# Kernel tuning notes

Hardware: AMD Instinct MI355X
Metric: run time of the kernel (lower is better)

The kernel has to match this reference:

```python
import jax, jax.numpy as jnp
import numpy as np
import math

N_HEAD = 12

def alibi_slopes(h):
    x = (2 ** 8) ** (1.0 / h)
    return jnp.array([1.0 / x ** (i + 1) for i in range(h)], dtype=jnp.float32)

def setup_inputs() -> dict:
    key = jax.random.key(0)
    k0, k1, k2 = jax.random.split(key, 3)
    B, T, C = 4, 2048, 576
    x = jax.random.normal(k0, (B, T, C), dtype=jnp.float32)
    w_qkv = jax.random.normal(k1, (3 * C, C), dtype=jnp.float32) * 0.02
    w_proj = jax.random.normal(k2, (C, C), dtype=jnp.float32) * 0.02
    return {"x": x, "w_qkv": w_qkv, "w_proj": w_proj}

def reference(x, w_qkv, w_proj):
    B, T, C = x.shape
    H = N_HEAD
    D = C // H
    qkv = x @ w_qkv.T  # [B,T,3C]
    q, k, v = jnp.split(qkv, 3, axis=2)
    q = q.reshape(B, T, H, D).transpose(0, 2, 1, 3)  # [B,H,T,D]
    k = k.reshape(B, T, H, D).transpose(0, 2, 1, 3)
    v = v.reshape(B, T, H, D).transpose(0, 2, 1, 3)
    # value residual with v1=None: v = 0.5*v + 0.5*v = v (faithful no-op)
    scale = 1.0 / math.sqrt(D)
    att = jnp.einsum('bhid,bhjd->bhij', q, k) * scale  # [B,H,T,T]
    # ALiBi bias as written: (col - row).clamp(min=0) * slope (zero on causal part)
    col = jnp.arange(T, dtype=jnp.float32)[None, :]
    row = jnp.arange(T, dtype=jnp.float32)[:, None]
    bias = jnp.maximum(col - row, 0.0)[None, :, :] * alibi_slopes(H)[:, None, None]  # [H,T,T]
    att = att + bias[None]
    causal = (jnp.arange(T)[None, :] <= jnp.arange(T)[:, None])  # [T,T] lower-tri
    att = jnp.where(causal[None, None], att, -jnp.inf)
    att = jax.nn.softmax(att, axis=-1)
    y = jnp.einsum('bhij,bhjd->bhid', att, v)  # [B,H,T,D]
    y = y.transpose(0, 2, 1, 3).reshape(B, T, C)
    return y @ w_proj.T
```

## Files before the change

### kernel.cpp

```cpp
#include <hip/hip_runtime.h>
#include <math.h>

#define Bn 4
#define Tn 2048
#define Cn 576
#define Hn 12
#define Dn 48
#define Mn (Bn*Tn)

#define QSCALE (1.4426950408889634f * 0.14433756729740643f)

typedef short  short8  __attribute__((ext_vector_type(8)));
typedef float  floatx4 __attribute__((ext_vector_type(4)));
typedef unsigned short ushort_t;
typedef unsigned short ushort8_t __attribute__((ext_vector_type(8)));

static __device__ __forceinline__ unsigned short f2bf(float f) {
    union { float f; unsigned int u; } v; v.f = f;
    unsigned int r = v.u + 0x7FFFu + ((v.u >> 16) & 1u);
    return (unsigned short)(r >> 16);
}

static __device__ __forceinline__ unsigned int pack_trunc(float a, float b) {
    union { float f; unsigned int u; } ua, ub; ua.f = a; ub.f = b;
    return (ua.u >> 16) | (ub.u & 0xFFFF0000u);
}

static __device__ __forceinline__ void gload16(void* lds, const void* g) {
    __builtin_amdgcn_global_load_lds(
        (const __attribute__((address_space(1))) void*)g,
        (__attribute__((address_space(3))) void*)lds, 16, 0, 0);
}

template<int N> static __device__ __forceinline__ void wait_vm_lg() {
    if constexpr (N == 0)
        asm volatile("s_waitcnt vmcnt(0) lgkmcnt(0)" ::: "memory");
    else if constexpr (N == 3)
        asm volatile("s_waitcnt vmcnt(3) lgkmcnt(0)" ::: "memory");
    else if constexpr (N == 5)
        asm volatile("s_waitcnt vmcnt(5) lgkmcnt(0)" ::: "memory");
    else if constexpr (N == 6)
        asm volatile("s_waitcnt vmcnt(6) lgkmcnt(0)" ::: "memory");
    else if constexpr (N == 10)
        asm volatile("s_waitcnt vmcnt(10) lgkmcnt(0)" ::: "memory");
    else
        static_assert(N == -12345, "unsupported waitcnt immediate");
}

__global__ __launch_bounds__(256)
void cast3(const float* __restrict__ a, ushort_t* __restrict__ oa, int na4,
           const float* __restrict__ b, ushort_t* __restrict__ ob, int nb4,
           const float* __restrict__ c, ushort_t* __restrict__ oc, int nc4)
{
    int i = blockIdx.x * 256 + threadIdx.x;
    const float* src; ushort_t* dst; int idx;
    if (i < na4)                  { src = a; dst = oa; idx = i; }
    else if (i < na4 + nb4)       { src = b; dst = ob; idx = i - na4; }
    else if (i < na4 + nb4 + nc4) { src = c; dst = oc; idx = i - na4 - nb4; }
    else return;
    float4 v = ((const float4*)src)[idx];
    ushort4 o;
    o.x = f2bf(v.x); o.y = f2bf(v.y); o.z = f2bf(v.z); o.w = f2bf(v.w);
    ((ushort4*)dst)[idx] = o;
}

template<int MODE, int MTILE>
__global__ __launch_bounds__(256)
void gemm_mfma(const ushort_t* __restrict__ A, const ushort_t* __restrict__ W,
               ushort_t* __restrict__ outb, float* __restrict__ outf)
{
    constexpr int SA   = MTILE / 16;
    constexpr int NSEG = SA + 4;
    constexpr int PW   = NSEG / 4;
    constexpr int MF   = MTILE / 64;
    constexpr int NB   = (MODE == 0) ? 27 : 9;
    constexpr int NST  = Cn / 32;
    constexpr int AH   = 3;
    constexpr int NBUF = 4;
    __shared__ __align__(16) ushort_t Ls[NBUF][NSEG][512];

    const int tid  = threadIdx.x;
    const int wave = tid >> 6;
    const int lane = tid & 63;
    const int m    = lane & 15;
    const int g    = lane >> 4;
    const int bid  = blockIdx.x;
    const int xcd  = bid & 7;
    const int slot = bid >> 3;
    const int n0   = (slot % NB) * 64;
    const int m0   = (xcd + 8 * (slot / NB)) * MTILE;

    floatx4 acc[MF][4];
    #pragma unroll
    for (int i = 0; i < MF; ++i)
        #pragma unroll
        for (int j = 0; j < 4; ++j)
            acc[i][j] = (floatx4){0.f, 0.f, 0.f, 0.f};

    const char* gp[PW];
    int         si[PW];
    #pragma unroll
    for (int i = 0; i < PW; ++i) {
        int s = wave + i * 4;
        si[i] = s;
        gp[i] = (s < SA)
            ? (const char*)(A + (size_t)(m0 + s * 16 + m) * Cn + g * 8)
            : (const char*)(W + (size_t)(n0 + (s - SA) * 16 + m) * Cn + g * 8);
    }

    #pragma unroll
    for (int s = 0; s < AH; ++s)
        #pragma unroll
        for (int i = 0; i < PW; ++i) { gload16(&Ls[s][si[i]][0], gp[i]); gp[i] += 64; }
    wait_vm_lg<(AH - 1) * PW>();
    __builtin_amdgcn_s_barrier();

    for (int j = 0; j < NST; ++j) {
        if (j + AH < NST) {
            #pragma unroll
            for (int i = 0; i < PW; ++i) {
                gload16(&Ls[(j + AH) & (NBUF - 1)][si[i]][0], gp[i]);
                gp[i] += 64;
            }
        }
        const int buf = j & (NBUF - 1);
        short8 bf4[4];
        #pragma unroll
        for (int jj = 0; jj < 4; ++jj)
            bf4[jj] = *(const short8*)&Ls[buf][SA + jj][lane * 8];
        #pragma unroll
        for (int i = 0; i < MF; ++i) {
            short8 af = *(const short8*)&Ls[buf][wave * MF + i][lane * 8];
            #pragma unroll
            for (int jj = 0; jj < 4; ++jj)
                acc[i][jj] = __builtin_amdgcn_mfma_f32_16x16x32_bf16(af, bf4[jj], acc[i][jj], 0, 0, 0);
        }
        if (j < NST - AH)        wait_vm_lg<(AH - 1) * PW>();
        else if (j == NST - AH)  wait_vm_lg<(AH - 2) * PW>();
        else                     wait_vm_lg<0>();
        __builtin_amdgcn_s_barrier();
    }

    const size_t per = (size_t)Bn * Hn * Tn * Dn;
    if (MODE == 0) {
        const int which = n0 / Cn;
        const int nb    = n0 - which * Cn;
        const int b     = m0 >> 11;
        const int t0g   = m0 & 2047;
        ushort_t* Lc = (ushort_t*)&Ls[0][0][0];
        if (which == 2) {
            constexpr int RS = MTILE + 8;
            #pragma unroll
            for (int i = 0; i < MF; ++i)
                #pragma unroll
                for (int j = 0; j < 4; ++j) {
                    ushort4 pk;
                    pk.x = f2bf(acc[i][j][0]); pk.y = f2bf(acc[i][j][1]);
                    pk.z = f2bf(acc[i][j][2]); pk.w = f2bf(acc[i][j][3]);
                    *(ushort4*)&Lc[(j * 16 + m) * RS + wave * (MTILE / 4) + i * 16 + g * 4] = pk;
                }
            __syncthreads();
            constexpr int CPC = MTILE / 8;
            constexpr int NIT = 64 * CPC / 256;
            #pragma unroll
            for (int it = 0; it < NIT; ++it) {
                int c    = tid + it * 256;
                int col  = c / CPC;
                int rowc = (c - col * CPC) * 8;
                int n    = nb + col;
                int h    = n / 48;
                int d    = n - h * 48;
                ushort_t* dst = outb + 2 * per
                    + (((size_t)(b * Hn + h) * Dn + d) * Tn) + t0g + rowc;
                *(ushort8_t*)dst = *(const ushort8_t*)&Lc[col * RS + rowc];
            }
        } else {
            const float sc = (which == 0) ? QSCALE : 1.0f;
            #pragma unroll
            for (int i = 0; i < MF; ++i)
                #pragma unroll
                for (int j = 0; j < 4; ++j)
                    #pragma unroll
                    for (int r = 0; r < 4; ++r)
                        Lc[(wave * (MTILE / 4) + i * 16 + g * 4 + r) * 80 + j * 16 + m] =
                            f2bf(acc[i][j][r] * sc);
            __syncthreads();
            constexpr int NIT = MTILE * 8 / 256;
            #pragma unroll
            for (int it = 0; it < NIT; ++it) {
                int c   = tid + it * 256;
                int row = c >> 3;
                int c8  = (c & 7) * 8;
                int n   = nb + c8;
                int h   = n / 48;
                int d   = n - h * 48;
                ushort_t* dst = outb + (size_t)which * per
                    + (((size_t)(b * Hn + h) * Tn + t0g + row) * Dn) + d;
                *(ushort8_t*)dst = *(const ushort8_t*)&Lc[row * 80 + c8];
            }
        }
    } else {
        #pragma unroll
        for (int i = 0; i < MF; ++i) {
            #pragma unroll
            for (int r = 0; r < 4; ++r) {
                int mrow = m0 + wave * (MTILE / 4) + i * 16 + g * 4 + r;
                #pragma unroll
                for (int j = 0; j < 4; ++j)
                    outf[(size_t)mrow * Cn + n0 + j * 16 + m] = acc[i][j][r];
            }
        }
    }
}

__global__ __launch_bounds__(512, 6)
void attn_mfma(const ushort_t* __restrict__ Q, const ushort_t* __restrict__ K,
               const ushort_t* __restrict__ V, ushort_t* __restrict__ Y,
               const ushort_t* __restrict__ zb)
{
    __shared__ __align__(16) ushort_t QPs[16][512];
    __shared__ __align__(16) ushort_t Ks[2][8][512];
    __shared__ __align__(16) ushort_t Vs[2][6][512];

    const int id   = blockIdx.x;
    const int kk   = id / 48;
    const int bh   = id - kk * 48;
    const int QT   = (kk & 1) ? (kk >> 1) : (15 - (kk >> 1));
    const int tid  = threadIdx.x;
    const int wave = tid >> 6;
    const int lane = tid & 63;
    const int m    = lane & 15;
    const int g    = lane >> 4;
    const int q0   = QT * 128;
    const int nkt  = 2 * QT + 2;

    const ushort_t* Qp = Q + (size_t)bh * Tn * Dn;
    const ushort_t* Kp = K + (size_t)bh * Tn * Dn;
    const ushort_t* Vp = V + (size_t)bh * Dn * Tn;

    {
        const char* qrp = (const char*)(Qp + (size_t)(q0 + wave * 16 + m) * Dn);
        gload16(&QPs[wave * 2 + 0][0], qrp + g * 16);
        gload16(&QPs[wave * 2 + 1][0], (g < 2) ? (qrp + 64 + g * 16) : (const char*)zb);
    }

    const bool  kpad = ((wave & 1) == 1) && (g >= 2);
    const char* kptr = kpad ? (const char*)zb
        : (const char*)(Kp + (size_t)((wave >> 1) * 16 + m) * Dn) + (wave & 1) * 64 + g * 16;
    const int   kadv = kpad ? 0 : 64 * Dn * 2;
    const char* vptr = (const char*)(Vp + (size_t)((wave >> 1) * 16 + m) * Tn)
                       + (wave & 1) * 64 + g * 16;
    const int   vadv = 64 * 2;

    gload16(&Ks[0][wave][0], kptr); kptr += kadv;
    if (wave < 6) { gload16(&Vs[0][wave][0], vptr); vptr += vadv; }
    __syncthreads();

    short8 bq[2];
    bq[0] = *(const short8*)&QPs[wave * 2 + 0][lane * 8];
    bq[1] = *(const short8*)&QPs[wave * 2 + 1][lane * 8];

    floatx4 acc[3];
    #pragma unroll
    for (int t = 0; t < 3; ++t) acc[t] = (floatx4){0.f, 0.f, 0.f, 0.f};
    float l_tot = 0.f;
    const int qrow  = q0 + wave * 16 + m;
    const int qwmin = q0 + wave * 16;
    const int qwmax = qwmin + 15;

    for (int jt = 0; jt < nkt; ++jt) {
        const int cur = jt & 1;
        const int j0  = jt * 64;
        if (jt + 1 < nkt) {
            gload16(&Ks[cur ^ 1][wave][0], kptr); kptr += kadv;
            if (wave < 6) { gload16(&Vs[cur ^ 1][wave][0], vptr); vptr += vadv; }
        }

        if (j0 <= qwmax) {
            floatx4 s[4];
            #pragma unroll
            for (int t = 0; t < 4; ++t) {
                s[t] = (floatx4){0.f, 0.f, 0.f, 0.f};
                #pragma unroll
                for (int kc = 0; kc < 2; ++kc) {
                    short8 ak = *(const short8*)&Ks[cur][t * 2 + kc][lane * 8];
                    s[t] = __builtin_amdgcn_mfma_f32_16x16x32_bf16(ak, bq[kc], s[t], 0, 0, 0);
                }
            }

            float p[4][4];
            float lsum = 0.f;
            if (j0 + 63 > qwmin) {
                #pragma unroll
                for (int t = 0; t < 4; ++t)
                    #pragma unroll
                    for (int r = 0; r < 4; ++r) {
                        int j = j0 + t * 16 + g * 4 + r;
                        float v = (j <= qrow) ? s[t][r] : -1e30f;
                        float e = __builtin_amdgcn_exp2f(v);
                        p[t][r] = e; lsum += e;
                    }
            } else {
                #pragma unroll
                for (int t = 0; t < 4; ++t)
                    #pragma unroll
                    for (int r = 0; r < 4; ++r) {
                        float e = __builtin_amdgcn_exp2f(s[t][r]);
                        p[t][r] = e; lsum += e;
                    }
            }
            lsum += __shfl_xor(lsum, 16);
            lsum += __shfl_xor(lsum, 32);
            l_tot += lsum;

            #pragma unroll
            for (int t = 0; t < 4; ++t) {
                uint2 w2;
                w2.x = pack_trunc(p[t][0], p[t][1]);
                w2.y = pack_trunc(p[t][2], p[t][3]);
                *(uint2*)&QPs[wave * 2 + (t >> 1)]
                             [(2 * (t & 1) + (g >> 1)) * 128 + m * 8 + (g & 1) * 4] = w2;
            }
            asm volatile("s_waitcnt lgkmcnt(0)" ::: "memory");

            #pragma unroll
            for (int kc = 0; kc < 2; ++kc) {
                short8 bp = *(const short8*)&QPs[wave * 2 + kc][lane * 8];
                #pragma unroll
                for (int t = 0; t < 3; ++t) {
                    short8 av = *(const short8*)&Vs[cur][t * 2 + kc][lane * 8];
                    acc[t] = __builtin_amdgcn_mfma_f32_16x16x32_bf16(av, bp, acc[t], 0, 0, 0);
                }
            }
        }

        __syncthreads();
    }

    const float inv = 1.0f / l_tot;
    const int b = bh / Hn;
    const int h = bh - b * Hn;
    ushort_t* yp = Y + ((size_t)(b * Tn + qrow)) * Cn + h * Dn;
    #pragma unroll
    for (int t = 0; t < 3; ++t) {
        ushort4 o;
        o.x = f2bf(acc[t][0] * inv);
        o.y = f2bf(acc[t][1] * inv);
        o.z = f2bf(acc[t][2] * inv);
        o.w = f2bf(acc[t][3] * inv);
        *(ushort4*)&yp[t * 16 + g * 4] = o;
    }
}

extern "C" void kernel_launch(void* const* d_in, const int* in_sizes, int n_in,
                              void* d_out, int out_size, void* d_ws, size_t ws_size,
                              hipStream_t stream)
{
    const float* x      = (const float*)d_in[0];
    const float* w_qkv  = (const float*)d_in[1];
    const float* w_proj = (const float*)d_in[2];
    float* out = (float*)d_out;

    const size_t per = (size_t)Bn * Hn * Tn * Dn;

    ushort_t* xb  = (ushort_t*)d_ws;
    ushort_t* wqb = xb  + (size_t)Mn * Cn;
    ushort_t* wpb = wqb + (size_t)3 * Cn * Cn;
    ushort_t* qkv = wpb + (size_t)Cn * Cn;
    ushort_t* yb  = qkv + 3 * per;
    ushort_t* zb  = yb  + (size_t)Mn * Cn;

    hipMemsetAsync(zb, 0, 256, stream);

    const int na4 = Mn * Cn / 4, nb4 = 3 * Cn * Cn / 4, nc4 = Cn * Cn / 4;
    cast3<<<dim3((na4 + nb4 + nc4 + 255) / 256), dim3(256), 0, stream>>>(
        x, xb, na4, w_qkv, wqb, nb4, w_proj, wpb, nc4);

    gemm_mfma<0, 256><<<dim3((Mn / 256) * 27), dim3(256), 0, stream>>>(xb, wqb, qkv, nullptr);

    attn_mfma<<<dim3((Tn / 128) * Bn * Hn), dim3(512), 0, stream>>>(
        qkv, qkv + per, qkv + 2 * per, yb, zb);

    gemm_mfma<1, 128><<<dim3((Mn / 128) * 9), dim3(256), 0, stream>>>(yb, wpb, nullptr, out);
}
```

Baseline: 183.9 us.

## Add dedicated 256x256-tile QKV GEMM kernel with deep LDS pipeline

Replaces the generic 256x64-tile QKV projection with a dedicated 512-thread kernel that computes 256x256 output tiles. It uses an 8-slot LDS ring fed by direct global-to-LDS loads, with explicit vmcnt/lgkmcnt gating and barriers, and raises wave priority around MFMA bursts. The goal is more operand reuse per tile and better overlap of loads with matrix math. The N dimension is padded from 1728 to 1792, so the last tile reads past the end of the QKV weight buffer and computes unused columns, which are masked on store. The output kernel is simplified to the projection-only mode.

```diff
diff --git a/kernel.cpp b/kernel.cpp
--- a/kernel.cpp
+++ b/kernel.cpp
@@ -7,6 +7,7 @@
 #define Hn 12
 #define Dn 48
 #define Mn (Bn*Tn)
+#define NPAD 1792
 
 #define QSCALE (1.4426950408889634f * 0.14433756729740643f)
 
@@ -30,6 +31,20 @@
     __builtin_amdgcn_global_load_lds(
         (const __attribute__((address_space(1))) void*)g,
         (__attribute__((address_space(3))) void*)lds, 16, 0, 0);
+}
+
+template<int N> static __device__ __forceinline__ void vmgate() {
+    if constexpr (N == 0)      asm volatile("s_waitcnt vmcnt(0)" ::: "memory");
+    else if constexpr (N == 4) asm volatile("s_waitcnt vmcnt(4)" ::: "memory");
+    else if constexpr (N == 8) asm volatile("s_waitcnt vmcnt(8)" ::: "memory");
+}
+static __device__ __forceinline__ void lgk0() {
+    asm volatile("s_waitcnt lgkmcnt(0)" ::: "memory");
+}
+static __device__ __forceinline__ void barrier_fence() {
+    asm volatile("" ::: "memory");
+    __builtin_amdgcn_s_barrier();
+    asm volatile("" ::: "memory");
 }
 
 template<int N> static __device__ __forceinline__ void wait_vm_lg() {
@@ -37,12 +52,8 @@
         asm volatile("s_waitcnt vmcnt(0) lgkmcnt(0)" ::: "memory");
     else if constexpr (N == 3)
         asm volatile("s_waitcnt vmcnt(3) lgkmcnt(0)" ::: "memory");
-    else if constexpr (N == 5)
-        asm volatile("s_waitcnt vmcnt(5) lgkmcnt(0)" ::: "memory");
     else if constexpr (N == 6)
         asm volatile("s_waitcnt vmcnt(6) lgkmcnt(0)" ::: "memory");
-    else if constexpr (N == 10)
-        asm volatile("s_waitcnt vmcnt(10) lgkmcnt(0)" ::: "memory");
     else
         static_assert(N == -12345, "unsupported waitcnt immediate");
 }
@@ -64,6 +75,194 @@
     ((ushort4*)dst)[idx] = o;
 }
 
+__global__ __launch_bounds__(512)
+void gemm_qkv(const ushort_t* __restrict__ A, const ushort_t* __restrict__ W,
+              ushort_t* __restrict__ outb)
+{
+    __shared__ __align__(16) ushort_t Ls[8][8192];
+
+    const int tid  = threadIdx.x;
+    const int wave = tid >> 6;
+    const int lane = tid & 63;
+    const int m    = lane & 15;
+    const int g    = lane >> 4;
+    const int wr   = wave >> 2;
+    const int wn   = wave & 3;
+
+    const int bid  = blockIdx.x;
+    const int xcd  = bid & 7;
+    const int slot = bid >> 3;
+    const int ng   = slot % 7;
+    const int mg   = xcd + 8 * (slot / 7);
+    const int m0   = mg * 256;
+    const int n0g  = ng * 256;
+
+    const int srow = lane >> 2;
+    const int schk = (lane & 3) * 16;
+    const char* aS0 = (const char*)A + (size_t)(m0  + (wave*2+0)*16 + srow) * (Cn*2) + schk;
+    const char* aS1 = (const char*)A + (size_t)(m0  + (wave*2+1)*16 + srow) * (Cn*2) + schk;
+    const char* bS0 = (const char*)W + (size_t)(n0g + (wave*2+0)*16 + srow) * (Cn*2) + schk;
+    const char* bS1 = (const char*)W + (size_t)(n0g + (wave*2+1)*16 + srow) * (Cn*2) + schk;
+
+    const int aoff = (wr * 128 + m) * 64 + g * 16;
+    const int boff = (wn * 64  + m) * 64 + g * 16;
+
+    floatx4 acc[8][4];
+    #pragma unroll
+    for (int i = 0; i < 8; ++i)
+        #pragma unroll
+        for (int j = 0; j < 4; ++j)
+            acc[i][j] = (floatx4){0.f, 0.f, 0.f, 0.f};
+
+    short8 af[8], bf01[2], bf23[2];
+
+    auto stageA = [&](int s) {
+        gload16(&Ls[s][(wave*2+0)*512], aS0); aS0 += 64;
+        gload16(&Ls[s][(wave*2+1)*512], aS1); aS1 += 64;
+    };
+    auto stageB = [&](int s) {
+        gload16(&Ls[s][(wave*2+0)*512], bS0); bS0 += 64;
+        gload16(&Ls[s][(wave*2+1)*512], bS1); bS1 += 64;
+    };
+    auto loadA = [&](int s) {
+        const char* base = (const char*)&Ls[s][0] + aoff;
+        #pragma unroll
+        for (int mf = 0; mf < 8; ++mf) af[mf] = *(const short8*)(base + mf * 1024);
+    };
+    auto loadB = [&](int s, int nf0, short8 (&bf)[2]) {
+        const char* base = (const char*)&Ls[s][0] + boff;
+        bf[0] = *(const short8*)(base + (nf0 + 0) * 1024);
+        bf[1] = *(const short8*)(base + (nf0 + 1) * 1024);
+    };
+    auto mfma16 = [&](short8 (&bf)[2], int nf0) {
+        __builtin_amdgcn_s_setprio(1);
+        #pragma unroll
+        for (int mf = 0; mf < 8; ++mf) {
+            acc[mf][nf0]     = __builtin_amdgcn_mfma_f32_16x16x32_bf16(af[mf], bf[0], acc[mf][nf0],     0, 0, 0);
+            acc[mf][nf0 + 1] = __builtin_amdgcn_mfma_f32_16x16x32_bf16(af[mf], bf[1], acc[mf][nf0 + 1], 0, 0, 0);
+        }
+        __builtin_amdgcn_s_setprio(0);
+    };
+
+    stageA(0); stageB(1); stageA(2); stageB(3); stageA(4); stageB(5);
+    vmgate<8>();
+    barrier_fence();
+
+    #define QKV_TILE(s0, d0, d1, d2, d3, G1m, G3m) do {                         \
+        constexpr int A0 = (s0) & 7,      B0 = ((s0)+1) & 7;                    \
+        constexpr int A1 = ((s0)+2) & 7,  B1 = ((s0)+3) & 7;                    \
+        constexpr int S0 = ((s0)+6) & 7,  S1 = ((s0)+7) & 7;                    \
+        constexpr int S2 = ((s0)+8) & 7,  S3 = ((s0)+9) & 7;                    \
+                                                    \
+        loadA(A0); loadB(B0, 0, bf01);                                          \
+        if (d0) stageA(S0);                                                     \
+        barrier_fence(); lgk0();                                                \
+        mfma16(bf01, 0);                                                        \
+        barrier_fence();                                                        \
+                                                            \
+        loadB(B0, 2, bf23);                                                     \
+        if (d1) stageB(S1);                                                     \
+        barrier_fence(); lgk0();                                                \
+        mfma16(bf23, 2);                                                        \
+        vmgate<G1m>();                                                          \
+        barrier_fence();                                                        \
+                                                    \
+        loadA(A1); loadB(B1, 0, bf01);                                          \
+        if (d2) stageA(S2);                                                     \
+        barrier_fence(); lgk0();                                                \
+        mfma16(bf01, 0);                                                        \
+        barrier_fence();                                                        \
+                                                            \
+        loadB(B1, 2, bf23);                                                     \
+        if (d3) stageB(S3);                                                     \
+        barrier_fence(); lgk0();                                                \
+        mfma16(bf23, 2);                                                        \
+        vmgate<G3m>();                                                          \
+        barrier_fence();                                                        \
+    } while (0)
+
+    #pragma unroll 1
+    for (int tt = 0; tt < 3; ++tt) {
+        QKV_TILE(0, 1, 1, 1, 1, 8, 8);
+        QKV_TILE(4, 1, 1, 1, 1, 8, 8);
+    }
+    QKV_TILE(0, 1, 1, 1, 1, 8, 8);
+    QKV_TILE(4, 1, 1, 0, 0, 8, 4);
+    QKV_TILE(0, 0, 0, 0, 0, 0, -1);
+    #undef QKV_TILE
+
+    const size_t per = (size_t)Bn * Hn * Tn * Dn;
+    const int b  = m0 >> 11;
+    const int t0 = m0 & 2047;
+    ushort_t* Lc = (ushort_t*)&Ls[0][0];
+
+    #pragma unroll
+    for (int h2 = 0; h2 < 2; ++h2) {
+        const int  nbase = n0g + h2 * 128;
+        const bool vmode = (nbase >= 1152);
+        if ((wn >> 1) == h2) {
+            if (!vmode) {
+                #pragma unroll
+                for (int mf = 0; mf < 8; ++mf)
+                    #pragma unroll
+                    for (int nf = 0; nf < 4; ++nf) {
+                        const int  nfb = n0g + wn * 64 + nf * 16;
+                        const float sc = (nfb < 576) ? QSCALE : 1.0f;
+                        const int col = (wn & 1) * 64 + nf * 16 + m;
+                        const int rb  = wr * 128 + mf * 16 + g * 4;
+                        #pragma unroll
+                        for (int r = 0; r < 4; ++r)
+                            Lc[(rb + r) * 136 + col] = f2bf(acc[mf][nf][r] * sc);
+                    }
+            } else {
+                #pragma unroll
+                for (int mf = 0; mf < 8; ++mf)
+                    #pragma unroll
+                    for (int nf = 0; nf < 4; ++nf) {
+                        const int col = (wn & 1) * 64 + nf * 16 + m;
+                        const int rb  = wr * 128 + mf * 16 + g * 4;
+                        ushort4 pk;
+                        pk.x = f2bf(acc[mf][nf][0]); pk.y = f2bf(acc[mf][nf][1]);
+                        pk.z = f2bf(acc[mf][nf][2]); pk.w = f2bf(acc[mf][nf][3]);
+                        *(ushort4*)&Lc[col * 264 + rb] = pk;
+                    }
+            }
+        }
+        __syncthreads();
+        if (!vmode) {
+            #pragma unroll
+            for (int it = 0; it < 8; ++it) {
+                const int c   = tid + it * 512;
+                const int row = c >> 4;
+                const int c8  = (c & 15) * 8;
+                const int n   = nbase + c8;
+                const int which = (n >= 576);
+                const int nn  = n - which * 576;
+                const int h   = nn / 48, d = nn - h * 48;
+                ushort_t* dst = outb + (size_t)which * per
+                    + ((size_t)(b * Hn + h) * Tn + t0 + row) * Dn + d;
+                *(ushort8_t*)dst = *(const ushort8_t*)&Lc[row * 136 + c8];
+            }
+        } else {
+            #pragma unroll
+            for (int it = 0; it < 8; ++it) {
+                const int c   = tid + it * 512;
+                const int col = c >> 5;
+                const int rc  = (c & 31) * 8;
+                const int n   = nbase + col;
+                if (n < 1728) {
+                    const int dd = n - 1152;
+                    const int h  = dd / 48, d = dd - h * 48;
+                    ushort_t* dst = outb + 2 * per
+                        + ((size_t)(b * Hn + h) * Dn + d) * Tn + t0 + rc;
+                    *(ushort8_t*)dst = *(const ushort8_t*)&Lc[col * 264 + rc];
+                }
+            }
+        }
+        __syncthreads();
+    }
+}
+
 template<int MODE, int MTILE>
 __global__ __launch_bounds__(256)
 void gemm_mfma(const ushort_t* __restrict__ A, const ushort_t* __restrict__ W,
@@ -73,7 +272,7 @@
     constexpr int NSEG = SA + 4;
     constexpr int PW   = NSEG / 4;
     constexpr int MF   = MTILE / 64;
-    constexpr int NB   = (MODE == 0) ? 27 : 9;
+    constexpr int NB   = 9;
     constexpr int NST  = Cn / 32;
     constexpr int AH   = 3;
     constexpr int NBUF = 4;
@@ -130,10 +329,10 @@
             bf4[jj] = *(const short8*)&Ls[buf][SA + jj][lane * 8];
         #pragma unroll
         for (int i = 0; i < MF; ++i) {
-            short8 af = *(const short8*)&Ls[buf][wave * MF + i][lane * 8];
+            short8 afr = *(const short8*)&Ls[buf][wave * MF + i][lane * 8];
             #pragma unroll
             for (int jj = 0; jj < 4; ++jj)
-                acc[i][jj] = __builtin_amdgcn_mfma_f32_16x16x32_bf16(af, bf4[jj], acc[i][jj], 0, 0, 0);
+                acc[i][jj] = __builtin_amdgcn_mfma_f32_16x16x32_bf16(afr, bf4[jj], acc[i][jj], 0, 0, 0);
         }
         if (j < NST - AH)        wait_vm_lg<(AH - 1) * PW>();
         else if (j == NST - AH)  wait_vm_lg<(AH - 2) * PW>();
@@ -141,74 +340,14 @@
         __builtin_amdgcn_s_barrier();
     }
 
-    const size_t per = (size_t)Bn * Hn * Tn * Dn;
-    if (MODE == 0) {
-        const int which = n0 / Cn;
-        const int nb    = n0 - which * Cn;
-        const int b     = m0 >> 11;
-        const int t0g   = m0 & 2047;
-        ushort_t* Lc = (ushort_t*)&Ls[0][0][0];
-        if (which == 2) {
-            constexpr int RS = MTILE + 8;
-            #pragma unroll
-            for (int i = 0; i < MF; ++i)
-                #pragma unroll
-                for (int j = 0; j < 4; ++j) {
-                    ushort4 pk;
-                    pk.x = f2bf(acc[i][j][0]); pk.y = f2bf(acc[i][j][1]);
-                    pk.z = f2bf(acc[i][j][2]); pk.w = f2bf(acc[i][j][3]);
-                    *(ushort4*)&Lc[(j * 16 + m) * RS + wave * (MTILE / 4) + i * 16 + g * 4] = pk;
-                }
-            __syncthreads();
-            constexpr int CPC = MTILE / 8;
-            constexpr int NIT = 64 * CPC / 256;
-            #pragma unroll
-            for (int it = 0; it < NIT; ++it) {
-                int c    = tid + it * 256;
-                int col  = c / CPC;
-                int rowc = (c - col * CPC) * 8;
-                int n    = nb + col;
-                int h    = n / 48;
-                int d    = n - h * 48;
-                ushort_t* dst = outb + 2 * per
-                    + (((size_t)(b * Hn + h) * Dn + d) * Tn) + t0g + rowc;
-                *(ushort8_t*)dst = *(const ushort8_t*)&Lc[col * RS + rowc];
-            }
-        } else {
-            const float sc = (which == 0) ? QSCALE : 1.0f;
-            #pragma unroll
-            for (int i = 0; i < MF; ++i)
-                #pragma unroll
-                for (int j = 0; j < 4; ++j)
-                    #pragma unroll
-                    for (int r = 0; r < 4; ++r)
-                        Lc[(wave * (MTILE / 4) + i * 16 + g * 4 + r) * 80 + j * 16 + m] =
-                            f2bf(acc[i][j][r] * sc);
-            __syncthreads();
-            constexpr int NIT = MTILE * 8 / 256;
-            #pragma unroll
-            for (int it = 0; it < NIT; ++it) {
-                int c   = tid + it * 256;
-                int row = c >> 3;
-                int c8  = (c & 7) * 8;
-                int n   = nb + c8;
-                int h   = n / 48;
-                int d   = n - h * 48;
-                ushort_t* dst = outb + (size_t)which * per
-                    + (((size_t)(b * Hn + h) * Tn + t0g + row) * Dn) + d;
-                *(ushort8_t*)dst = *(const ushort8_t*)&Lc[row * 80 + c8];
-            }
-        }
-    } else {
-        #pragma unroll
-        for (int i = 0; i < MF; ++i) {
-            #pragma unroll
-            for (int r = 0; r < 4; ++r) {
-                int mrow = m0 + wave * (MTILE / 4) + i * 16 + g * 4 + r;
-                #pragma unroll
-                for (int j = 0; j < 4; ++j)
-                    outf[(size_t)mrow * Cn + n0 + j * 16 + m] = acc[i][j][r];
-            }
+    #pragma unroll
+    for (int i = 0; i < MF; ++i) {
+        #pragma unroll
+        for (int r = 0; r < 4; ++r) {
+            int mrow = m0 + wave * (MTILE / 4) + i * 16 + g * 4 + r;
+            #pragma unroll
+            for (int j = 0; j < 4; ++j)
+                outf[(size_t)mrow * Cn + n0 + j * 16 + m] = acc[i][j][r];
         }
     }
 }
@@ -376,7 +515,7 @@
     cast3<<<dim3((na4 + nb4 + nc4 + 255) / 256), dim3(256), 0, stream>>>(
         x, xb, na4, w_qkv, wqb, nb4, w_proj, wpb, nc4);
 
-    gemm_mfma<0, 256><<<dim3((Mn / 256) * 27), dim3(256), 0, stream>>>(xb, wqb, qkv, nullptr);
+    gemm_qkv<<<dim3(224), dim3(512), 0, stream>>>(xb, wqb, qkv);
 
     attn_mfma<<<dim3((Tn / 128) * Bn * Hn), dim3(512), 0, stream>>>(
         qkv, qkv + per, qkv + 2 * per, yb, zb);
```

Result: faster. 163.4 us (-11.2%).
